# Performance work log

Hardware: AMD Instinct MI355X
Metric: run time of the kernel (lower is better)

## Reference

```python
import jax, jax.numpy as jnp
import numpy as np

B, D, L = 16384, 1024, 4

def setup_inputs() -> dict:
    key = jax.random.key(0)
    k1, k2 = jax.random.split(key)
    inputs = jax.random.normal(k1, (B, D), dtype=jnp.float32)
    # xavier_uniform for (D, 1): bound = sqrt(6/(D+1))
    bound = float(np.sqrt(6.0 / (D + 1)))
    weights = jax.random.uniform(k2, (L, D), dtype=jnp.float32, minval=-bound, maxval=bound)
    biases = jnp.zeros((L, D), dtype=jnp.float32)
    return {"inputs": inputs, "weights": weights, "biases": biases}

def reference(inputs, weights, biases):
    # inputs: [B, D]; weights/biases: [L, D]
    x0 = inputs

    def step(x, wb):
        w, b = wb
        xw = jnp.einsum("bd,d->b", x, w)          # x^T w  -> [B]
        x_next = x0 * xw[:, None] + b[None, :] + x  # outer product + bias + residual
        return x_next, None

    out, _ = jax.lax.scan(step, x0, (weights, biases))
    return out
```

## Files before the change

### kernel.cpp

```cpp
#include <hip/hip_runtime.h>


#define NB 16384
#define ND 1024
#define NL 4

__global__ __launch_bounds__(256) void crossnet_scalars(
    const float* __restrict__ W,
    const float* __restrict__ Bias,
    float* __restrict__ ws) {
  __shared__ float red1[256];
  __shared__ float red2[256];
  __shared__ float red3[256];
  const int t = threadIdx.x;

  const float4* B4 = (const float4*)Bias;
  const float4* W4 = (const float4*)W;
  float4 b0 = B4[0 * 256 + t];
  float4 b1 = B4[1 * 256 + t];
  float4 b2 = B4[2 * 256 + t];
  float4 b3 = B4[3 * 256 + t];
  float4 w1 = W4[1 * 256 + t];
  float4 w2 = W4[2 * 256 + t];
  float4 w3 = W4[3 * 256 + t];

  float ux = b0.x, uy = b0.y, uz = b0.z, uw = b0.w;
  float s1 = ux * w1.x + uy * w1.y + uz * w1.z + uw * w1.w;
  ux += b1.x; uy += b1.y; uz += b1.z; uw += b1.w;
  float s2 = ux * w2.x + uy * w2.y + uz * w2.z + uw * w2.w;
  ux += b2.x; uy += b2.y; uz += b2.z; uw += b2.w;
  float s3 = ux * w3.x + uy * w3.y + uz * w3.z + uw * w3.w;
  ux += b3.x; uy += b3.y; uz += b3.z; uw += b3.w;

  float4 u4v; u4v.x = ux; u4v.y = uy; u4v.z = uz; u4v.w = uw;
  ((float4*)(ws + 4))[t] = u4v;

  red1[t] = s1; red2[t] = s2; red3[t] = s3;
  __syncthreads();
  for (int off = 128; off >= 1; off >>= 1) {
    if (t < off) {
      red1[t] += red1[t + off];
      red2[t] += red2[t + off];
      red3[t] += red3[t + off];
    }
    __syncthreads();
  }
  if (t == 0) {
    ws[0] = 0.0f;
    ws[1] = red1[0];
    ws[2] = red2[0];
    ws[3] = red3[0];
  }
}

__global__ __launch_bounds__(256) void crossnet_main(
    const float* __restrict__ X,
    const float* __restrict__ W,
    const float* __restrict__ ws,
    float* __restrict__ Out) {
  const int wave = threadIdx.x >> 6;
  const int lane = threadIdx.x & 63;
  const int row = blockIdx.x * 4 + wave;

  const float4* X4 = (const float4*)X + (size_t)row * 256;
  float4* O4 = (float4*)Out + (size_t)row * 256;
  const float4* W4 = (const float4*)W;

  float4 x0, x1, x2, x3;
  x0 = X4[lane];
  x1 = X4[lane + 64];
  x2 = X4[lane + 128];
  x3 = X4[lane + 192];

  float p0 = 0.f, p1 = 0.f, p2 = 0.f, p3 = 0.f;
#define DOT4(acc, xv, wv) \
  acc += (xv).x * (wv).x + (xv).y * (wv).y + (xv).z * (wv).z + (xv).w * (wv).w
#pragma unroll
  for (int k = 0; k < 4; ++k) {
    const float4 xv = (k == 0) ? x0 : (k == 1) ? x1 : (k == 2) ? x2 : x3;
    const int idx = lane + 64 * k;
    float4 w0v = W4[0 * 256 + idx];
    float4 w1v = W4[1 * 256 + idx];
    float4 w2v = W4[2 * 256 + idx];
    float4 w3v = W4[3 * 256 + idx];
    DOT4(p0, xv, w0v);
    DOT4(p1, xv, w1v);
    DOT4(p2, xv, w2v);
    DOT4(p3, xv, w3v);
  }
#undef DOT4

#pragma unroll
  for (int off = 32; off >= 1; off >>= 1) {
    p0 += __shfl_xor(p0, off, 64);
    p1 += __shfl_xor(p1, off, 64);
    p2 += __shfl_xor(p2, off, 64);
    p3 += __shfl_xor(p3, off, 64);
  }

  const float s0 = ws[0], s1 = ws[1], s2 = ws[2], s3 = ws[3];
  float c = 1.0f;
  c = c * (p0 + 1.0f) + s0;
  c = c * (p1 + 1.0f) + s1;
  c = c * (p2 + 1.0f) + s2;
  c = c * (p3 + 1.0f) + s3;

  const float4* U4 = (const float4*)(ws + 4);
#pragma unroll
  for (int k = 0; k < 4; ++k) {
    const float4 xv = (k == 0) ? x0 : (k == 1) ? x1 : (k == 2) ? x2 : x3;
    const int idx = lane + 64 * k;
    float4 u = U4[idx];
    float4 o;
    o.x = c * xv.x + u.x;
    o.y = c * xv.y + u.y;
    o.z = c * xv.z + u.z;
    o.w = c * xv.w + u.w;
    O4[idx] = o;
  }
}

extern "C" void kernel_launch(void* const* d_in, const int* in_sizes, int n_in,
                              void* d_out, int out_size, void* d_ws, size_t ws_size,
                              hipStream_t stream) {
  const float* X = (const float*)d_in[0];
  const float* W = (const float*)d_in[1];
  const float* Bias = (const float*)d_in[2];
  float* Out = (float*)d_out;
  float* ws = (float*)d_ws;

  crossnet_scalars<<<1, 256, 0, stream>>>(W, Bias, ws);
  crossnet_main<<<NB / 4, 256, 0, stream>>>(X, W, ws, Out);
}
```

Before: 30.89 us.

## Fuse bias-scalar precompute into main kernel and process four rows per wave

Drops the separate single-block scalar kernel. Each block now recomputes the bias-derived vector u and the three bias·weight scalars itself, holding them in LDS with wave-shuffle reductions. Each wave handles four rows and keeps all weight vectors in registers, so per-row weight reloads are avoided and there is one fewer launch and no global workspace round trip. The cost is redundant scalar work in every block, higher register pressure, and a quarter as many blocks.

```diff
diff --git a/kernel.cpp b/kernel.cpp
--- a/kernel.cpp
+++ b/kernel.cpp
@@ -2,121 +2,117 @@
 
 
 #define NB 16384
-#define ND 1024
-#define NL 4
+#define ROWS_PER_WAVE 4
+#define NWAVES 4
+#define ROWS_PER_BLOCK (ROWS_PER_WAVE * NWAVES)
+#define NBLOCKS (NB / ROWS_PER_BLOCK)
 
-__global__ __launch_bounds__(256) void crossnet_scalars(
+#define DOT4(a, b) ((a).x*(b).x + (a).y*(b).y + (a).z*(b).z + (a).w*(b).w)
+
+__global__ __launch_bounds__(256, 4) void crossnet_fused(
+    const float* __restrict__ X,
     const float* __restrict__ W,
     const float* __restrict__ Bias,
-    float* __restrict__ ws) {
-  __shared__ float red1[256];
-  __shared__ float red2[256];
-  __shared__ float red3[256];
+    float* __restrict__ Out) {
+  __shared__ float4 lds_u4[256];
+  __shared__ float lds_s[NWAVES][3];
+
   const int t = threadIdx.x;
+  const int wave = t >> 6;
+  const int lane = t & 63;
 
+  const float4* W4 = (const float4*)W;
   const float4* B4 = (const float4*)Bias;
-  const float4* W4 = (const float4*)W;
-  float4 b0 = B4[0 * 256 + t];
-  float4 b1 = B4[1 * 256 + t];
-  float4 b2 = B4[2 * 256 + t];
-  float4 b3 = B4[3 * 256 + t];
-  float4 w1 = W4[1 * 256 + t];
-  float4 w2 = W4[2 * 256 + t];
-  float4 w3 = W4[3 * 256 + t];
 
-  float ux = b0.x, uy = b0.y, uz = b0.z, uw = b0.w;
-  float s1 = ux * w1.x + uy * w1.y + uz * w1.z + uw * w1.w;
-  ux += b1.x; uy += b1.y; uz += b1.z; uw += b1.w;
-  float s2 = ux * w2.x + uy * w2.y + uz * w2.z + uw * w2.w;
-  ux += b2.x; uy += b2.y; uz += b2.z; uw += b2.w;
-  float s3 = ux * w3.x + uy * w3.y + uz * w3.z + uw * w3.w;
-  ux += b3.x; uy += b3.y; uz += b3.z; uw += b3.w;
+  float4 b0 = B4[t];
+  float4 b1 = B4[256 + t];
+  float4 b2 = B4[512 + t];
+  float4 b3 = B4[768 + t];
+  float4 w1t = W4[256 + t];
+  float4 w2t = W4[512 + t];
+  float4 w3t = W4[768 + t];
 
-  float4 u4v; u4v.x = ux; u4v.y = uy; u4v.z = uz; u4v.w = uw;
-  ((float4*)(ws + 4))[t] = u4v;
-
-  red1[t] = s1; red2[t] = s2; red3[t] = s3;
-  __syncthreads();
-  for (int off = 128; off >= 1; off >>= 1) {
-    if (t < off) {
-      red1[t] += red1[t + off];
-      red2[t] += red2[t + off];
-      red3[t] += red3[t + off];
-    }
-    __syncthreads();
-  }
-  if (t == 0) {
-    ws[0] = 0.0f;
-    ws[1] = red1[0];
-    ws[2] = red2[0];
-    ws[3] = red3[0];
-  }
-}
-
-__global__ __launch_bounds__(256) void crossnet_main(
-    const float* __restrict__ X,
-    const float* __restrict__ W,
-    const float* __restrict__ ws,
-    float* __restrict__ Out) {
-  const int wave = threadIdx.x >> 6;
-  const int lane = threadIdx.x & 63;
-  const int row = blockIdx.x * 4 + wave;
-
-  const float4* X4 = (const float4*)X + (size_t)row * 256;
-  float4* O4 = (float4*)Out + (size_t)row * 256;
-  const float4* W4 = (const float4*)W;
-
-  float4 x0, x1, x2, x3;
-  x0 = X4[lane];
-  x1 = X4[lane + 64];
-  x2 = X4[lane + 128];
-  x3 = X4[lane + 192];
-
-  float p0 = 0.f, p1 = 0.f, p2 = 0.f, p3 = 0.f;
-#define DOT4(acc, xv, wv) \
-  acc += (xv).x * (wv).x + (xv).y * (wv).y + (xv).z * (wv).z + (xv).w * (wv).w
-#pragma unroll
-  for (int k = 0; k < 4; ++k) {
-    const float4 xv = (k == 0) ? x0 : (k == 1) ? x1 : (k == 2) ? x2 : x3;
-    const int idx = lane + 64 * k;
-    float4 w0v = W4[0 * 256 + idx];
-    float4 w1v = W4[1 * 256 + idx];
-    float4 w2v = W4[2 * 256 + idx];
-    float4 w3v = W4[3 * 256 + idx];
-    DOT4(p0, xv, w0v);
-    DOT4(p1, xv, w1v);
-    DOT4(p2, xv, w2v);
-    DOT4(p3, xv, w3v);
-  }
-#undef DOT4
+  float4 u = b0;
+  float s1p = DOT4(u, w1t);
+  u.x += b1.x; u.y += b1.y; u.z += b1.z; u.w += b1.w;
+  float s2p = DOT4(u, w2t);
+  u.x += b2.x; u.y += b2.y; u.z += b2.z; u.w += b2.w;
+  float s3p = DOT4(u, w3t);
+  u.x += b3.x; u.y += b3.y; u.z += b3.z; u.w += b3.w;
+  lds_u4[t] = u;
 
 #pragma unroll
   for (int off = 32; off >= 1; off >>= 1) {
-    p0 += __shfl_xor(p0, off, 64);
-    p1 += __shfl_xor(p1, off, 64);
-    p2 += __shfl_xor(p2, off, 64);
-    p3 += __shfl_xor(p3, off, 64);
+    s1p += __shfl_xor(s1p, off, 64);
+    s2p += __shfl_xor(s2p, off, 64);
+    s3p += __shfl_xor(s3p, off, 64);
+  }
+  if (lane == 0) {
+    lds_s[wave][0] = s1p;
+    lds_s[wave][1] = s2p;
+    lds_s[wave][2] = s3p;
   }
 
-  const float s0 = ws[0], s1 = ws[1], s2 = ws[2], s3 = ws[3];
-  float c = 1.0f;
-  c = c * (p0 + 1.0f) + s0;
-  c = c * (p1 + 1.0f) + s1;
-  c = c * (p2 + 1.0f) + s2;
-  c = c * (p3 + 1.0f) + s3;
+  float4 w[4][4];
+#pragma unroll
+  for (int l = 0; l < 4; ++l)
+#pragma unroll
+    for (int k = 0; k < 4; ++k)
+      w[l][k] = W4[l * 256 + lane + 64 * k];
 
-  const float4* U4 = (const float4*)(ws + 4);
+  __syncthreads();
+
+  const float s1 = lds_s[0][0] + lds_s[1][0] + lds_s[2][0] + lds_s[3][0];
+  const float s2 = lds_s[0][1] + lds_s[1][1] + lds_s[2][1] + lds_s[3][1];
+  const float s3 = lds_s[0][2] + lds_s[1][2] + lds_s[2][2] + lds_s[3][2];
+
+  float4 u4r[4];
 #pragma unroll
-  for (int k = 0; k < 4; ++k) {
-    const float4 xv = (k == 0) ? x0 : (k == 1) ? x1 : (k == 2) ? x2 : x3;
-    const int idx = lane + 64 * k;
-    float4 u = U4[idx];
-    float4 o;
-    o.x = c * xv.x + u.x;
-    o.y = c * xv.y + u.y;
-    o.z = c * xv.z + u.z;
-    o.w = c * xv.w + u.w;
-    O4[idx] = o;
+  for (int k = 0; k < 4; ++k) u4r[k] = lds_u4[lane + 64 * k];
+
+  const int row0 = blockIdx.x * ROWS_PER_BLOCK + wave * ROWS_PER_WAVE;
+#pragma unroll
+  for (int r = 0; r < ROWS_PER_WAVE; ++r) {
+    const int row = row0 + r;
+    const float4* Xr = (const float4*)X + (size_t)row * 256;
+    float4* Or = (float4*)Out + (size_t)row * 256;
+
+    float4 x[4];
+#pragma unroll
+    for (int k = 0; k < 4; ++k) x[k] = Xr[lane + 64 * k];
+
+    float p0 = 0.f, p1 = 0.f, p2 = 0.f, p3 = 0.f;
+#pragma unroll
+    for (int k = 0; k < 4; ++k) {
+      p0 += DOT4(x[k], w[0][k]);
+      p1 += DOT4(x[k], w[1][k]);
+      p2 += DOT4(x[k], w[2][k]);
+      p3 += DOT4(x[k], w[3][k]);
+    }
+
+#pragma unroll
+    for (int off = 32; off >= 1; off >>= 1) {
+      p0 += __shfl_xor(p0, off, 64);
+      p1 += __shfl_xor(p1, off, 64);
+      p2 += __shfl_xor(p2, off, 64);
+      p3 += __shfl_xor(p3, off, 64);
+    }
+
+    float c = 1.0f;
+    c = c * (p0 + 1.0f);
+    c = c * (p1 + 1.0f) + s1;
+    c = c * (p2 + 1.0f) + s2;
+    c = c * (p3 + 1.0f) + s3;
+
+#pragma unroll
+    for (int k = 0; k < 4; ++k) {
+      float4 o;
+      o.x = c * x[k].x + u4r[k].x;
+      o.y = c * x[k].y + u4r[k].y;
+      o.z = c * x[k].z + u4r[k].z;
+      o.w = c * x[k].w + u4r[k].w;
+      Or[lane + 64 * k] = o;
+    }
   }
 }
 
@@ -127,8 +123,6 @@
   const float* W = (const float*)d_in[1];
   const float* Bias = (const float*)d_in[2];
   float* Out = (float*)d_out;
-  float* ws = (float*)d_ws;
 
-  crossnet_scalars<<<1, 256, 0, stream>>>(W, Bias, ws);
-  crossnet_main<<<NB / 4, 256, 0, stream>>>(X, W, ws, Out);
+  crossnet_fused<<<NBLOCKS, 256, 0, stream>>>(X, W, Bias, Out);
 }
```

After: 28.80 us. 1.07x faster.
